# Performance work log

Measured on AMD Instinct MI355X. Metric: run time of the kernel, lower is better.

Reference implementation:

```python
import jax, jax.numpy as jnp
import numpy as np

LATENT_DIM = 768

def setup_inputs() -> dict:
    key = jax.random.key(0)
    k1, k2 = jax.random.split(key)
    x_latent = jax.random.normal(k1, (16, 4096, LATENT_DIM), dtype=jnp.float32)
    prompts_latent = jax.random.normal(k2, (16, 64, LATENT_DIM), dtype=jnp.float32)
    return {"x_latent": x_latent, "prompts_latent": prompts_latent}

def reference(x_latent, prompts_latent):
    # Base class: get_tokens / get_query are identity in the base math.
    tokens = x_latent            # [b, n, d]
    q = prompts_latent           # [b, p, d]
    scale = LATENT_DIM ** (-0.5)
    # [b, p, n] scores
    attn = jnp.einsum('bpd,bnd->bpn', q, tokens) * scale
    attn = jax.nn.softmax(attn, axis=-1)
    # [b, p, d] context
    context = jnp.einsum('bpn,bnd->bpd', attn, tokens)
    return context
```

## Files before the change

### kernel.cpp

```cpp
#include <hip/hip_runtime.h>
#include <hip/hip_bf16.h>

#define BB 16
#define PP 64
#define NN 4096
#define DD 768
#define TT 16
#define NTILE 16

typedef __attribute__((ext_vector_type(4))) float f32x4;
typedef __attribute__((ext_vector_type(8))) __bf16 bf16x8;
typedef __attribute__((ext_vector_type(2))) __bf16 bf16x2;
typedef __attribute__((ext_vector_type(4))) _Float16 f16x4;

__device__ __forceinline__ f32x4 mfma16(bf16x8 a, bf16x8 b, f32x4 c) {
    return __builtin_amdgcn_mfma_f32_16x16x32_bf16(a, b, c, 0, 0, 0);
}

__device__ __forceinline__ void gl_lds(const float* g, float* l) {
    __builtin_amdgcn_global_load_lds(
        (const __attribute__((address_space(1))) void*)g,
        (__attribute__((address_space(3))) void*)l, 16, 0, 0);
}

#define S_WAITCNT_VM(N) asm volatile("s_waitcnt vmcnt(" #N ")" ::: "memory")
#define BARRIER() do { __builtin_amdgcn_s_barrier(); asm volatile("" ::: "memory"); } while (0)
#define LDS_BARRIER() do { asm volatile("s_waitcnt lgkmcnt(0)" ::: "memory"); \
                           __builtin_amdgcn_s_barrier(); \
                           __builtin_amdgcn_sched_barrier(0); } while (0)

#define SM_BYTES 141056

__global__ __launch_bounds__(512, 2) void k_flash(const float* __restrict__ x,
                                                  const float* __restrict__ q,
                                                  float* __restrict__ statm,
                                                  float* __restrict__ statl,
                                                  _Float16* __restrict__ part) {
    const int b  = blockIdx.x >> 4;
    const int sp = blockIdx.x & 15;
    const int n0 = sp * 256;

    __shared__ __align__(16) char smem[SM_BYTES];
    float*  vst  = (float*)smem;
    float*  lpf  = (float*)(smem + 98304);
    __bf16* pbuf = (__bf16*)(smem + 135168);
    float*  mrun = (float*)(smem + 140288);
    float*  lrun = (float*)(smem + 140544);
    float*  rsc  = (float*)(smem + 140800);

    const int t = threadIdx.x;
    const int w = t >> 6, lane = t & 63;
    const int l15 = lane & 15, hi = lane >> 4;

    const size_t xbase = (size_t)b * NN + n0;
    const size_t qbase = (size_t)b * PP;

    bf16x8 qf[4][3];
    #pragma unroll
    for (int am = 0; am < 4; ++am)
        #pragma unroll
        for (int s = 0; s < 3; ++s) {
            const size_t off = (qbase + am * 16 + l15) * DD + w * 96 + s * 32 + hi * 8;
            const float4 a = *(const float4*)&q[off];
            const float4 c = *(const float4*)&q[off + 4];
            qf[am][s] = (bf16x8){(__bf16)a.x, (__bf16)a.y, (__bf16)a.z, (__bf16)a.w,
                                 (__bf16)c.x, (__bf16)c.y, (__bf16)c.z, (__bf16)c.w};
        }

    for (int i = t; i < 64 * 20; i += 512) ((unsigned*)pbuf)[i] = 0;
    if (t < 64) { mrun[t] = -1e30f; lrun[t] = 0.f; }

    f32x4 O[4][6] = {};

#define STAGE(bufi, tile) do {                                                \
        float* vb_ = vst + (bufi) * (TT * DD);                                \
        _Pragma("unroll")                                                     \
        for (int i_ = 0; i_ < 6; ++i_) {                                      \
            const int idx_ = w * 6 + i_;                                      \
            const int r_   = idx_ / 3;                                        \
            const int gg_  = (((idx_ % 3) << 6) + lane) ^ (r_ & 7);           \
            gl_lds(&x[(xbase + (size_t)(tile) * TT + r_) * DD + (size_t)gg_ * 4], \
                   vb_ + idx_ * 256);                                         \
        }                                                                     \
    } while (0)

    STAGE(0, 0);

    const float scale = 0.036084391824351615f;
    const int p_  = t >> 3;
    const int np_ = t & 7;

    for (int tile = 0; tile < NTILE; ++tile) {
        if (tile < NTILE - 1) { STAGE((tile + 1) & 1, tile + 1); S_WAITCNT_VM(6); }
        else                  { S_WAITCNT_VM(0); }
        BARRIER();
        const float* vb = vst + (tile & 1) * (TT * DD);

        f32x4 acc[4] = {};
        #pragma unroll
        for (int s = 0; s < 3; ++s) {
            const int g0 = w * 24 + s * 8 + hi * 2;
            const int ky = l15 & 7;
            const f32x4 lo = *(const f32x4*)(vb + l15 * DD + ((g0 ^ ky) << 2));
            const f32x4 hg = *(const f32x4*)(vb + l15 * DD + (((g0 + 1) ^ ky) << 2));
            const bf16x8 kf = {(__bf16)lo[0], (__bf16)lo[1], (__bf16)lo[2], (__bf16)lo[3],
                               (__bf16)hg[0], (__bf16)hg[1], (__bf16)hg[2], (__bf16)hg[3]};
            #pragma unroll
            for (int am = 0; am < 4; ++am) acc[am] = mfma16(qf[am][s], kf, acc[am]);
        }
        #pragma unroll
        for (int am = 0; am < 4; ++am)
            #pragma unroll
            for (int j = 0; j < 4; ++j)
                lpf[(w * 64 + am * 16 + hi * 4 + j) * 18 + l15] = acc[am][j];
        LDS_BARRIER();

        float s0 = 0.f, s1 = 0.f;
        #pragma unroll
        for (int sl = 0; sl < 8; ++sl) {
            const float2 v2 = *(const float2*)&lpf[(sl * 64 + p_) * 18 + 2 * np_];
            s0 += v2.x; s1 += v2.y;
        }
        s0 *= scale; s1 *= scale;
        float mt = fmaxf(s0, s1);
        mt = fmaxf(mt, __shfl_xor(mt, 1));
        mt = fmaxf(mt, __shfl_xor(mt, 2));
        mt = fmaxf(mt, __shfl_xor(mt, 4));
        const float mo = mrun[p_];
        const float mn = fmaxf(mo, mt);
        const float e0 = __expf(s0 - mn), e1 = __expf(s1 - mn);
        float lsum = e0 + e1;
        lsum += __shfl_xor(lsum, 1);
        lsum += __shfl_xor(lsum, 2);
        lsum += __shfl_xor(lsum, 4);
        *(bf16x2*)&pbuf[p_ * 40 + 2 * np_] = (bf16x2){(__bf16)e0, (__bf16)e1};
        if (np_ == 0) {
            const float f = __expf(mo - mn);
            lrun[p_] = lrun[p_] * f + lsum;
            mrun[p_] = mn;
            rsc[p_]  = f;
        }
        LDS_BARRIER();

        #pragma unroll
        for (int am = 0; am < 4; ++am)
            #pragma unroll
            for (int j = 0; j < 4; ++j) {
                const float f = rsc[am * 16 + hi * 4 + j];
                #pragma unroll
                for (int df = 0; df < 6; ++df) O[am][df][j] *= f;
            }

        bf16x8 pf[4];
        #pragma unroll
        for (int am = 0; am < 4; ++am)
            pf[am] = *(const bf16x8*)&pbuf[(am * 16 + l15) * 40 + hi * 8];
        #pragma unroll
        for (int df = 0; df < 6; ++df) {
            const int d_ = w * 96 + df * 16 + l15;
            const int gd = d_ >> 2, dw = d_ & 3;
            float vf[8];
            #pragma unroll
            for (int i = 0; i < 8; ++i) {
                const int k_ = (hi * 8 + i) & 15;
                vf[i] = vb[k_ * DD + ((gd ^ i) << 2) + dw];
            }
            const bf16x8 vfr = {(__bf16)vf[0], (__bf16)vf[1], (__bf16)vf[2], (__bf16)vf[3],
                                (__bf16)vf[4], (__bf16)vf[5], (__bf16)vf[6], (__bf16)vf[7]};
            #pragma unroll
            for (int am = 0; am < 4; ++am) O[am][df] = mfma16(pf[am], vfr, O[am][df]);
        }
        LDS_BARRIER();
    }

    if (t < 64) {
        const size_t si = ((size_t)b * 16 + sp) * 64 + t;
        statm[si] = mrun[t];
        statl[si] = lrun[t];
    }
    #pragma unroll
    for (int am = 0; am < 4; ++am)
        #pragma unroll
        for (int j = 0; j < 4; ++j) {
            const int p = am * 16 + hi * 4 + j;
            #pragma unroll
            for (int df = 0; df < 6; ++df) {
                const int d_ = w * 96 + df * 16 + l15;
                part[(((size_t)sp * BB + b) * PP + p) * DD + d_] = (_Float16)O[am][df][j];
            }
        }
}

__global__ __launch_bounds__(256) void k_combine(const _Float16* __restrict__ part,
                                                 const float* __restrict__ statm,
                                                 const float* __restrict__ statl,
                                                 float* __restrict__ out) {
    const size_t idx = (size_t)blockIdx.x * 256 + threadIdx.x;
    const size_t e = idx * 4;
    const int bp = (int)(e / DD);
    const int b = bp >> 6, p = bp & 63;

    float M = -1e30f;
    #pragma unroll
    for (int c = 0; c < 16; ++c) M = fmaxf(M, statm[((size_t)b * 16 + c) * 64 + p]);
    float Ee[16];
    float D = 0.f;
    #pragma unroll
    for (int c = 0; c < 16; ++c) {
        Ee[c] = __expf(statm[((size_t)b * 16 + c) * 64 + p] - M);
        D += Ee[c] * statl[((size_t)b * 16 + c) * 64 + p];
    }
    const float inv = 1.f / D;

    float4 v = {0.f, 0.f, 0.f, 0.f};
    #pragma unroll
    for (int c = 0; c < 16; ++c) {
        const f16x4 h = *(const f16x4*)&part[(size_t)c * ((size_t)BB * PP * DD) + e];
        v.x += Ee[c] * (float)h[0];
        v.y += Ee[c] * (float)h[1];
        v.z += Ee[c] * (float)h[2];
        v.w += Ee[c] * (float)h[3];
    }
    v.x *= inv; v.y *= inv; v.z *= inv; v.w *= inv;
    *(float4*)&out[e] = v;
}

extern "C" void kernel_launch(void* const* d_in, const int* in_sizes, int n_in,
                              void* d_out, int out_size, void* d_ws, size_t ws_size,
                              hipStream_t stream) {
    const float* x = (const float*)d_in[0];
    const float* q = (const float*)d_in[1];
    float* out = (float*)d_out;

    char* ws = (char*)d_ws;
    float*     statm = (float*)ws;
    float*     statl = (float*)(ws + 65536);
    _Float16*  part  = (_Float16*)(ws + 131072);

    hipLaunchKernelGGL(k_flash,   dim3(256), dim3(512), 0, stream, x, q, statm, statl, part);
    hipLaunchKernelGGL(k_combine, dim3(768), dim3(256), 0, stream, part, statm, statl, out);
}
```

Measured before the change: 69.51 us.

## Stage X tiles as bf16 in LDS with register prefetch and larger tiles

Replaces the direct global-to-LDS fp32 staging with register loads of the next tile. These are converted to bf16 and written into a padded, swizzled LDS buffer after the softmax phase. The tile size doubles to 32 rows (8 iterations), which halves the barriers per row and lets the fp32-to-bf16 conversion happen once per element instead of in both matmuls. The per-wave partial score buffer is replaced by LDS atomicAdd reduction, and O rescaling is skipped when all factors are 1. This trades extra register pressure and LDS atomics for less LDS traffic, less conversion work and fewer synchronisation points.

```diff
diff --git a/kernel.cpp b/kernel.cpp
--- a/kernel.cpp
+++ b/kernel.cpp
@@ -5,31 +5,24 @@
 #define PP 64
 #define NN 4096
 #define DD 768
-#define TT 16
-#define NTILE 16
+#define TT 32
+#define NTILE 8
+#define BFROW 776
 
 typedef __attribute__((ext_vector_type(4))) float f32x4;
 typedef __attribute__((ext_vector_type(8))) __bf16 bf16x8;
-typedef __attribute__((ext_vector_type(2))) __bf16 bf16x2;
+typedef __attribute__((ext_vector_type(4))) __bf16 bf16x4;
 typedef __attribute__((ext_vector_type(4))) _Float16 f16x4;
 
 __device__ __forceinline__ f32x4 mfma16(bf16x8 a, bf16x8 b, f32x4 c) {
     return __builtin_amdgcn_mfma_f32_16x16x32_bf16(a, b, c, 0, 0, 0);
 }
 
-__device__ __forceinline__ void gl_lds(const float* g, float* l) {
-    __builtin_amdgcn_global_load_lds(
-        (const __attribute__((address_space(1))) void*)g,
-        (__attribute__((address_space(3))) void*)l, 16, 0, 0);
-}
-
-#define S_WAITCNT_VM(N) asm volatile("s_waitcnt vmcnt(" #N ")" ::: "memory")
-#define BARRIER() do { __builtin_amdgcn_s_barrier(); asm volatile("" ::: "memory"); } while (0)
 #define LDS_BARRIER() do { asm volatile("s_waitcnt lgkmcnt(0)" ::: "memory"); \
                            __builtin_amdgcn_s_barrier(); \
                            __builtin_amdgcn_sched_barrier(0); } while (0)
 
-#define SM_BYTES 141056
+#define SM_BYTES 114432
 
 __global__ __launch_bounds__(512, 2) void k_flash(const float* __restrict__ x,
                                                   const float* __restrict__ q,
@@ -41,18 +34,18 @@
     const int n0 = sp * 256;
 
     __shared__ __align__(16) char smem[SM_BYTES];
-    float*  vst  = (float*)smem;
-    float*  lpf  = (float*)(smem + 98304);
-    __bf16* pbuf = (__bf16*)(smem + 135168);
-    float*  mrun = (float*)(smem + 140288);
-    float*  lrun = (float*)(smem + 140544);
-    float*  rsc  = (float*)(smem + 140800);
+    __bf16* vbf  = (__bf16*)smem;
+    float*  lpf  = (float*)(smem + 99328);
+    __bf16* pbuf = (__bf16*)(smem + 108544);
+    float*  mrun = (float*)(smem + 113664);
+    float*  lrun = (float*)(smem + 113920);
+    float*  rsc  = (float*)(smem + 114176);
 
     const int t = threadIdx.x;
     const int w = t >> 6, lane = t & 63;
     const int l15 = lane & 15, hi = lane >> 4;
 
-    const size_t xbase = (size_t)b * NN + n0;
+    const float* xp = x + ((size_t)b * NN + n0) * DD;
     const size_t qbase = (size_t)b * PP;
 
     bf16x8 qf[4][3];
@@ -67,73 +60,97 @@
                                  (__bf16)c.x, (__bf16)c.y, (__bf16)c.z, (__bf16)c.w};
         }
 
-    for (int i = t; i < 64 * 20; i += 512) ((unsigned*)pbuf)[i] = 0;
-    if (t < 64) { mrun[t] = -1e30f; lrun[t] = 0.f; }
-
-    f32x4 O[4][6] = {};
-
-#define STAGE(bufi, tile) do {                                                \
-        float* vb_ = vst + (bufi) * (TT * DD);                                \
+    int srcOff[12], dstOff[12];
+    #pragma unroll
+    for (int i = 0; i < 12; ++i) {
+        const int c = i * 8 + w;
+        const int r = c / 3;
+        const int colf = (c % 3) * 256 + lane * 4;
+        srcOff[i] = r * DD + colf;
+        dstOff[i] = r * BFROW + (colf ^ (((r >> 3) & 3) << 4));
+    }
+
+#define VLOAD(tile) do {                                                      \
+        const float* sp_ = xp + (size_t)(tile) * (TT * DD);                   \
         _Pragma("unroll")                                                     \
-        for (int i_ = 0; i_ < 6; ++i_) {                                      \
-            const int idx_ = w * 6 + i_;                                      \
-            const int r_   = idx_ / 3;                                        \
-            const int gg_  = (((idx_ % 3) << 6) + lane) ^ (r_ & 7);           \
-            gl_lds(&x[(xbase + (size_t)(tile) * TT + r_) * DD + (size_t)gg_ * 4], \
-                   vb_ + idx_ * 256);                                         \
+        for (int i_ = 0; i_ < 12; ++i_)                                       \
+            tv[i_] = *(const float4*)(sp_ + srcOff[i_]);                      \
+    } while (0)
+
+#define VWRITE(bb) do {                                                       \
+        __bf16* vb_ = vbf + (bb) * (TT * BFROW);                              \
+        _Pragma("unroll")                                                     \
+        for (int i_ = 0; i_ < 12; ++i_) {                                     \
+            bf16x4 h = {(__bf16)tv[i_].x, (__bf16)tv[i_].y,                   \
+                        (__bf16)tv[i_].z, (__bf16)tv[i_].w};                  \
+            *(bf16x4*)&vb_[dstOff[i_]] = h;                                   \
         }                                                                     \
     } while (0)
 
-    STAGE(0, 0);
+    for (int i = t; i < 64 * 36; i += 512) lpf[i] = 0.f;
+    if (t < 64) { mrun[t] = -1e30f; lrun[t] = 0.f; }
+    float4 tv[12];
+    VLOAD(0);
+    VWRITE(0);
+    LDS_BARRIER();
+
+    f32x4 O[4][6] = {};
 
     const float scale = 0.036084391824351615f;
     const int p_  = t >> 3;
     const int np_ = t & 7;
 
-    for (int tile = 0; tile < NTILE; ++tile) {
-        if (tile < NTILE - 1) { STAGE((tile + 1) & 1, tile + 1); S_WAITCNT_VM(6); }
-        else                  { S_WAITCNT_VM(0); }
-        BARRIER();
-        const float* vb = vst + (tile & 1) * (TT * DD);
-
-        f32x4 acc[4] = {};
+    #pragma unroll 1
+    for (int tl = 0; tl < NTILE; ++tl) {
+        __bf16* vb = vbf + (tl & 1) * (TT * BFROW);
+
+        if (tl < NTILE - 1) VLOAD(tl + 1);
+        __builtin_amdgcn_sched_barrier(0);
+
+        f32x4 acc[4][2] = {};
         #pragma unroll
         for (int s = 0; s < 3; ++s) {
-            const int g0 = w * 24 + s * 8 + hi * 2;
-            const int ky = l15 & 7;
-            const f32x4 lo = *(const f32x4*)(vb + l15 * DD + ((g0 ^ ky) << 2));
-            const f32x4 hg = *(const f32x4*)(vb + l15 * DD + (((g0 + 1) ^ ky) << 2));
-            const bf16x8 kf = {(__bf16)lo[0], (__bf16)lo[1], (__bf16)lo[2], (__bf16)lo[3],
-                               (__bf16)hg[0], (__bf16)hg[1], (__bf16)hg[2], (__bf16)hg[3]};
-            #pragma unroll
-            for (int am = 0; am < 4; ++am) acc[am] = mfma16(qf[am][s], kf, acc[am]);
+            bf16x8 kf[2];
+            #pragma unroll
+            for (int an = 0; an < 2; ++an) {
+                const int row = an * 16 + l15;
+                const int col = (w * 96 + s * 32 + hi * 8) ^ (((row >> 3) & 3) << 4);
+                kf[an] = *(const bf16x8*)&vb[row * BFROW + col];
+            }
+            #pragma unroll
+            for (int am = 0; am < 4; ++am)
+                #pragma unroll
+                for (int an = 0; an < 2; ++an)
+                    acc[am][an] = mfma16(qf[am][s], kf[an], acc[am][an]);
         }
         #pragma unroll
         for (int am = 0; am < 4; ++am)
             #pragma unroll
-            for (int j = 0; j < 4; ++j)
-                lpf[(w * 64 + am * 16 + hi * 4 + j) * 18 + l15] = acc[am][j];
+            for (int an = 0; an < 2; ++an)
+                #pragma unroll
+                for (int j = 0; j < 4; ++j)
+                    atomicAdd(&lpf[(am * 16 + hi * 4 + j) * 36 + an * 16 + l15],
+                              acc[am][an][j]);
         LDS_BARRIER();
 
-        float s0 = 0.f, s1 = 0.f;
-        #pragma unroll
-        for (int sl = 0; sl < 8; ++sl) {
-            const float2 v2 = *(const float2*)&lpf[(sl * 64 + p_) * 18 + 2 * np_];
-            s0 += v2.x; s1 += v2.y;
-        }
-        s0 *= scale; s1 *= scale;
-        float mt = fmaxf(s0, s1);
+        const f32x4 sv = *(const f32x4*)&lpf[p_ * 36 + np_ * 4];
+        const float s0 = sv[0] * scale, s1 = sv[1] * scale,
+                    s2 = sv[2] * scale, s3 = sv[3] * scale;
+        float mt = fmaxf(fmaxf(s0, s1), fmaxf(s2, s3));
         mt = fmaxf(mt, __shfl_xor(mt, 1));
         mt = fmaxf(mt, __shfl_xor(mt, 2));
         mt = fmaxf(mt, __shfl_xor(mt, 4));
         const float mo = mrun[p_];
         const float mn = fmaxf(mo, mt);
         const float e0 = __expf(s0 - mn), e1 = __expf(s1 - mn);
-        float lsum = e0 + e1;
+        const float e2 = __expf(s2 - mn), e3 = __expf(s3 - mn);
+        float lsum = e0 + e1 + e2 + e3;
         lsum += __shfl_xor(lsum, 1);
         lsum += __shfl_xor(lsum, 2);
         lsum += __shfl_xor(lsum, 4);
-        *(bf16x2*)&pbuf[p_ * 40 + 2 * np_] = (bf16x2){(__bf16)e0, (__bf16)e1};
+        *(bf16x4*)&pbuf[p_ * 40 + np_ * 4] =
+            (bf16x4){(__bf16)e0, (__bf16)e1, (__bf16)e2, (__bf16)e3};
+        *(f32x4*)&lpf[p_ * 36 + np_ * 4] = (f32x4){0.f, 0.f, 0.f, 0.f};
         if (np_ == 0) {
             const float f = __expf(mo - mn);
             lrun[p_] = lrun[p_] * f + lsum;
@@ -142,14 +159,21 @@
         }
         LDS_BARRIER();
 
-        #pragma unroll
-        for (int am = 0; am < 4; ++am)
-            #pragma unroll
-            for (int j = 0; j < 4; ++j) {
-                const float f = rsc[am * 16 + hi * 4 + j];
+        if (tl < NTILE - 1) VWRITE((tl + 1) & 1);
+
+        #pragma unroll
+        for (int am = 0; am < 4; ++am) {
+            float f[4];
+            #pragma unroll
+            for (int j = 0; j < 4; ++j) f[j] = rsc[am * 16 + hi * 4 + j];
+            const bool nz = (f[0] != 1.f) | (f[1] != 1.f) | (f[2] != 1.f) | (f[3] != 1.f);
+            if (__any(nz)) {
                 #pragma unroll
-                for (int df = 0; df < 6; ++df) O[am][df][j] *= f;
+                for (int df = 0; df < 6; ++df)
+                    #pragma unroll
+                    for (int j = 0; j < 4; ++j) O[am][df][j] *= f[j];
             }
+        }
 
         bf16x8 pf[4];
         #pragma unroll
@@ -157,18 +181,14 @@
             pf[am] = *(const bf16x8*)&pbuf[(am * 16 + l15) * 40 + hi * 8];
         #pragma unroll
         for (int df = 0; df < 6; ++df) {
-            const int d_ = w * 96 + df * 16 + l15;
-            const int gd = d_ >> 2, dw = d_ & 3;
-            float vf[8];
-            #pragma unroll
-            for (int i = 0; i < 8; ++i) {
-                const int k_ = (hi * 8 + i) & 15;
-                vf[i] = vb[k_ * DD + ((gd ^ i) << 2) + dw];
-            }
-            const bf16x8 vfr = {(__bf16)vf[0], (__bf16)vf[1], (__bf16)vf[2], (__bf16)vf[3],
-                                (__bf16)vf[4], (__bf16)vf[5], (__bf16)vf[6], (__bf16)vf[7]};
-            #pragma unroll
-            for (int am = 0; am < 4; ++am) O[am][df] = mfma16(pf[am], vfr, O[am][df]);
+            const int dcol = (w * 96 + df * 16 + l15) ^ (hi << 4);
+            bf16x8 vfr;
+            #pragma unroll
+            for (int i = 0; i < 8; ++i)
+                vfr[i] = vb[(hi * 8 + i) * BFROW + dcol];
+            #pragma unroll
+            for (int am = 0; am < 4; ++am)
+                O[am][df] = mfma16(pf[am], vfr, O[am][df]);
         }
         LDS_BARRIER();
     }
```

Result: slower. 267.5 us (+284.8%).
